# Performance work log

Hardware: AMD Instinct MI355X
Metric: run time of the kernel (lower is better)

Reference implementation:

```python
import jax, jax.numpy as jnp
import numpy as np

B, T, H, K = 64, 512, 768, 11
START_ID, END_ID = 9, 10  # tag_to_ix['<CLS>'], tag_to_ix['<SEP>']
NEG = -10000.0


def setup_inputs() -> dict:
    key = jax.random.key(0)
    k1, k2, k3, k4 = jax.random.split(key, 4)
    embeds = jax.random.normal(k1, (B, T, H), dtype=jnp.float32)
    W_fc = jax.random.normal(k2, (K, H), dtype=jnp.float32) * 0.02
    b_fc = jax.random.normal(k3, (K,), dtype=jnp.float32) * 0.02
    transitions = jax.random.normal(k4, (K, K), dtype=jnp.float32)
    # __init__ masking: no transition out of anything into START row, none into END col
    transitions = transitions.at[START_ID, :].set(NEG)
    transitions = transitions.at[:, END_ID].set(NEG)
    return {"embeds": embeds, "W_fc": W_fc, "b_fc": b_fc, "transitions": transitions}


def reference(embeds, W_fc, b_fc, transitions):
    # fc projection: feats[b,t,k] (PLM_crf path: encoder output -> Linear)
    feats = jnp.einsum('bth,kh->btk', embeds, W_fc) + b_fc  # [B,T,K]
    Bv, Tv, Kv = feats.shape

    # Viterbi: log_delta init -10000 except start tag; NOTE the original never
    # adds feats[:, 0] (loop starts at t=1), so we faithfully skip it too.
    log_delta0 = jnp.full((Bv, Kv), NEG, dtype=feats.dtype).at[:, START_ID].set(0.0)

    def step(log_delta, feat_t):
        # transitions[i, j]: score of moving from prev tag j to tag i
        scores = transitions[None, :, :] + log_delta[:, None, :]  # [B,K,K]
        psi_t = jnp.argmax(scores, axis=-1)                       # [B,K] best prev tag
        log_delta_new = jnp.max(scores, axis=-1) + feat_t         # [B,K]
        return log_delta_new, psi_t

    feats_seq = jnp.swapaxes(feats[:, 1:], 0, 1)                  # [T-1,B,K]
    log_delta, psi = jax.lax.scan(step, log_delta0, feats_seq)    # psi: [T-1,B,K]

    score = jnp.max(log_delta, axis=-1)                           # [B]
    last_tag = jnp.argmax(log_delta, axis=-1)                     # [B]

    # Backtrack: path[t] = psi[t+1][path[t+1]] for t = T-2 .. 0
    def back(next_tag, psi_t):
        tag = jnp.take_along_axis(psi_t, next_tag[:, None], axis=-1)[:, 0]
        return tag, tag

    _, path_rest = jax.lax.scan(back, last_tag, psi, reverse=True)  # [T-1,B]
    path = jnp.concatenate([jnp.swapaxes(path_rest, 0, 1), last_tag[:, None]], axis=1)  # [B,T]
    return score, path
```

## Files before the change

### kernel.cpp

```cpp
#include <hip/hip_runtime.h>

#define BB 64
#define TT 512
#define HH 768
#define KK 11
#define START_ID 9
#define NEGV -10000.0f
#define TT4 (TT + 4)
#define NROWS 16

typedef float vf2 __attribute__((ext_vector_type(2)));

__device__ __forceinline__ float ninf() { return __int_as_float(0xff800000); }

template <int CTRL>
__device__ __forceinline__ float dpp_add(float x) {
    int yi = __builtin_amdgcn_update_dpp(0, __float_as_int(x), CTRL, 0xF, 0xF, false);
    return x + __int_as_float(yi);
}

__device__ __forceinline__ float wave_sum_to_lane63(float x) {
    x = dpp_add<0x111>(x);
    x = dpp_add<0x112>(x);
    x = dpp_add<0x114>(x);
    x = dpp_add<0x118>(x);
    x = dpp_add<0x142>(x);
    x = dpp_add<0x143>(x);
    return x;
}

__device__ __forceinline__ float rlane(float v, int l) {
    return __int_as_float(__builtin_amdgcn_readlane(__float_as_int(v), l));
}

template <int PAT>
__device__ __forceinline__ float quad_fmax(float x) {
    int yi = __builtin_amdgcn_update_dpp(0, __float_as_int(x), PAT, 0xF, 0xF, false);
    return fmaxf(x, __int_as_float(yi));
}

__global__ __launch_bounds__(256) void fc_kernel(const float* __restrict__ embeds,
                                                 const float* __restrict__ W,
                                                 const float* __restrict__ bias,
                                                 float* __restrict__ feats) {
    __shared__ __align__(16) float w_lds[KK * HH];

    const int tid = threadIdx.x;
    const int lane = tid & 63;

    {
        const float4* src = reinterpret_cast<const float4*>(W);
        float4* dst = reinterpret_cast<float4*>(w_lds);
#pragma unroll
        for (int i = 0; i < 9; ++i) {
            int idx = tid + i * 256;
            if (idx < KK * HH / 4) dst[idx] = src[idx];
        }
    }

    float bk[KK];
#pragma unroll
    for (int k = 0; k < KK; ++k) bk[k] = bias[k];

    __syncthreads();

    const int wave_id = (blockIdx.x * blockDim.x + tid) >> 6;
    const int base = wave_id * 8;
    const int lo = lane * 4;

    const float* ea = embeds + (size_t)base * HH;
    const float* eb = ea + HH;
    float4 a0 = *reinterpret_cast<const float4*>(ea + 0   + lo);
    float4 a1 = *reinterpret_cast<const float4*>(ea + 256 + lo);
    float4 a2 = *reinterpret_cast<const float4*>(ea + 512 + lo);
    float4 b0 = *reinterpret_cast<const float4*>(eb + 0   + lo);
    float4 b1 = *reinterpret_cast<const float4*>(eb + 256 + lo);
    float4 b2 = *reinterpret_cast<const float4*>(eb + 512 + lo);

#pragma unroll 1
    for (int rr = 0; rr < 8; rr += 2) {
        const int nrr = (rr + 2) & 7;
        const float* na = embeds + (size_t)(base + nrr) * HH;
        const float* nb = na + HH;
        float4 na0 = *reinterpret_cast<const float4*>(na + 0   + lo);
        float4 na1 = *reinterpret_cast<const float4*>(na + 256 + lo);
        float4 na2 = *reinterpret_cast<const float4*>(na + 512 + lo);
        float4 nb0 = *reinterpret_cast<const float4*>(nb + 0   + lo);
        float4 nb1 = *reinterpret_cast<const float4*>(nb + 256 + lo);
        float4 nb2 = *reinterpret_cast<const float4*>(nb + 512 + lo);

        vf2 va[6] = {{a0.x, a0.y}, {a0.z, a0.w}, {a1.x, a1.y},
                     {a1.z, a1.w}, {a2.x, a2.y}, {a2.z, a2.w}};
        vf2 vb[6] = {{b0.x, b0.y}, {b0.z, b0.w}, {b1.x, b1.y},
                     {b1.z, b1.w}, {b2.x, b2.y}, {b2.z, b2.w}};

        float4 w0 = *reinterpret_cast<const float4*>(w_lds + 0 + lo);
        float4 w1 = *reinterpret_cast<const float4*>(w_lds + 256 + lo);
        float4 w2 = *reinterpret_cast<const float4*>(w_lds + 512 + lo);

        float rA[KK], rB[KK];
#pragma unroll
        for (int k = 0; k < KK; ++k) {
            const int nk = (k == KK - 1) ? 0 : k + 1;
            float4 nw0 = *reinterpret_cast<const float4*>(w_lds + nk * HH + 0 + lo);
            float4 nw1 = *reinterpret_cast<const float4*>(w_lds + nk * HH + 256 + lo);
            float4 nw2 = *reinterpret_cast<const float4*>(w_lds + nk * HH + 512 + lo);

            vf2 wv[6] = {{w0.x, w0.y}, {w0.z, w0.w},
                         {w1.x, w1.y}, {w1.z, w1.w},
                         {w2.x, w2.y}, {w2.z, w2.w}};
            vf2 sA = va[0] * wv[0];
            vf2 sB = vb[0] * wv[0];
#pragma unroll
            for (int r = 1; r < 6; ++r) { sA += va[r] * wv[r]; sB += vb[r] * wv[r]; }
            rA[k] = wave_sum_to_lane63(sA.x + sA.y);
            rB[k] = wave_sum_to_lane63(sB.x + sB.y);

            w0 = nw0; w1 = nw1; w2 = nw2;
        }

        if (lane == 63) {
            float* oA = feats + (size_t)(base + rr) * KK;
#pragma unroll
            for (int k = 0; k < KK; ++k) oA[k] = rA[k] + bk[k];
#pragma unroll
            for (int k = 0; k < KK; ++k) oA[KK + k] = rB[k] + bk[k];
        }

        a0 = na0; a1 = na1; a2 = na2;
        b0 = nb0; b1 = nb1; b2 = nb2;
    }
}

__global__ __launch_bounds__(256) void viterbi_kernel(const float* __restrict__ feats,
                                                      const float* __restrict__ trans,
                                                      float* __restrict__ out) {
    __shared__ __align__(16) float featsT[NROWS * TT4];
    __shared__ __align__(16) float dh[(TT - 1) * 12 + 16];
    __shared__ int psi_lds[(TT - 1) * KK];
    __shared__ float tr_lds[KK * KK];
    __shared__ int comp[15 * KK];
    __shared__ int bt[16];
    __shared__ int sh_last;

    const int tid = threadIdx.x;
    const int b = blockIdx.x;

    {
        const float4* src = reinterpret_cast<const float4*>(feats + (size_t)b * TT * KK);
        for (int idx4 = tid; idx4 < TT * KK / 4; idx4 += 256) {
            float4 v = src[idx4];
            const int e = idx4 * 4;
#pragma unroll
            for (int u = 0; u < 4; ++u) {
                int t = (e + u) / KK;
                int k = (e + u) - t * KK;
                if (t > 0) featsT[k * TT4 + (t - 1)] = (&v.x)[u];
            }
        }
        for (int x = tid; x < (NROWS - KK) * TT4; x += 256)
            featsT[KK * TT4 + x] = ninf();
        if (tid < KK * KK) tr_lds[tid] = trans[tid];
    }
    __syncthreads();

    if (tid < 64) {
        const int i = tid >> 2;
        const int q = tid & 3;

        float trq0, trq1, trq2;
        {
            const int j0 = 3 * q, j1 = 3 * q + 1, j2 = 3 * q + 2;
            trq0 = (i < KK && j0 < KK) ? tr_lds[i * KK + j0] : 0.0f;
            trq1 = (i < KK && j1 < KK) ? tr_lds[i * KK + j1] : 0.0f;
            trq2 = (i < KK && j2 < KK) ? tr_lds[i * KK + j2] : 0.0f;
        }
        const int a0 = 48 * q, a1 = 48 * q + 16, a2 = 48 * q + 32;

        float delta = (i == START_ID) ? 0.0f : ((i < KK) ? NEGV : ninf());

        auto vstep = [&](float fcur, float& hs) {
            hs = delta;
            const int di = __float_as_int(delta);
            float d0 = __int_as_float(__builtin_amdgcn_ds_bpermute(a0, di));
            float d1 = __int_as_float(__builtin_amdgcn_ds_bpermute(a1, di));
            float d2 = __int_as_float(__builtin_amdgcn_ds_bpermute(a2, di));
            float m = fmaxf(fmaxf(trq0 + d0, trq1 + d1), trq2 + d2);
            m = quad_fmax<0xB1>(m);
            m = quad_fmax<0x4E>(m);
            delta = m + fcur;
        };

        const float* frow = featsT + i * TT4;
        float* dwbase = dh + i;

        float h0, h1, h2, h3, h4, h5, h6, h7;
        float h8, h9, h10, h11, h12, h13, h14, h15;

        float4 A0 = *reinterpret_cast<const float4*>(frow + 0);
        float4 A1 = *reinterpret_cast<const float4*>(frow + 4);
        float4 A2 = *reinterpret_cast<const float4*>(frow + 8);
        float4 A3 = *reinterpret_cast<const float4*>(frow + 12);

#pragma unroll 1
        for (int c = 0; c < 31; ++c) {
            const float* nf = frow + (c + 1) * 16;
            float4 B0 = *reinterpret_cast<const float4*>(nf + 0);
            float4 B1 = *reinterpret_cast<const float4*>(nf + 4);
            float4 B2 = *reinterpret_cast<const float4*>(nf + 8);
            float4 B3 = *reinterpret_cast<const float4*>(nf + 12);

            vstep(A0.x, h0);  vstep(A0.y, h1);  vstep(A0.z, h2);  vstep(A0.w, h3);
            vstep(A1.x, h4);  vstep(A1.y, h5);  vstep(A1.z, h6);  vstep(A1.w, h7);
            vstep(A2.x, h8);  vstep(A2.y, h9);  vstep(A2.z, h10); vstep(A2.w, h11);
            vstep(A3.x, h12); vstep(A3.y, h13); vstep(A3.z, h14); vstep(A3.w, h15);

            if (q == 0 && i < KK) {
                float* dw = dwbase + c * 192;
                dw[0]   = h0;  dw[12]  = h1;  dw[24]  = h2;  dw[36]  = h3;
                dw[48]  = h4;  dw[60]  = h5;  dw[72]  = h6;  dw[84]  = h7;
                dw[96]  = h8;  dw[108] = h9;  dw[120] = h10; dw[132] = h11;
                dw[144] = h12; dw[156] = h13; dw[168] = h14; dw[180] = h15;
            }

            A0 = B0; A1 = B1; A2 = B2; A3 = B3;
        }
        vstep(A0.x, h0);  vstep(A0.y, h1);  vstep(A0.z, h2);  vstep(A0.w, h3);
        vstep(A1.x, h4);  vstep(A1.y, h5);  vstep(A1.z, h6);  vstep(A1.w, h7);
        vstep(A2.x, h8);  vstep(A2.y, h9);  vstep(A2.z, h10); vstep(A2.w, h11);
        vstep(A3.x, h12); vstep(A3.y, h13); vstep(A3.z, h14);
        if (q == 0 && i < KK) {
            float* dw = dwbase + 31 * 192;
            dw[0]   = h0;  dw[12]  = h1;  dw[24]  = h2;  dw[36]  = h3;
            dw[48]  = h4;  dw[60]  = h5;  dw[72]  = h6;  dw[84]  = h7;
            dw[96]  = h8;  dw[108] = h9;  dw[120] = h10; dw[132] = h11;
            dw[144] = h12; dw[156] = h13; dw[168] = h14;
        }

        float dfin[KK];
#pragma unroll
        for (int j = 0; j < KK; ++j) dfin[j] = rlane(delta, 4 * j);
        float best = dfin[0];
        int last = 0;
#pragma unroll
        for (int j = 1; j < KK; ++j) {
            bool c = dfin[j] > best;
            best = c ? dfin[j] : best;
            last = c ? j : last;
        }
        if (tid == 0) {
            out[b] = best;
            out[BB + (size_t)b * TT + (TT - 1)] = (float)last;
            sh_last = last;
        }
    }
    __syncthreads();

    {
        const int i = tid & 15;
        const int sg = tid >> 4;
        if (i < KK) {
            float tri[KK];
#pragma unroll
            for (int j = 0; j < KK; ++j) tri[j] = tr_lds[i * KK + j];
            for (int s = sg; s < TT - 1; s += 16) {
                const float4* dr = reinterpret_cast<const float4*>(dh + s * 12);
                float4 a = dr[0], c4 = dr[1], d4 = dr[2];
                float sc[KK] = {tri[0] + a.x,  tri[1] + a.y,  tri[2] + a.z,  tri[3] + a.w,
                                tri[4] + c4.x, tri[5] + c4.y, tri[6] + c4.z, tri[7] + c4.w,
                                tri[8] + d4.x, tri[9] + d4.y, tri[10] + d4.z};
                float bv = sc[0];
                int bj = 0;
#pragma unroll
                for (int j = 1; j < KK; ++j) {
                    bool c = sc[j] > bv;
                    bv = c ? sc[j] : bv;
                    bj = c ? j : bj;
                }
                psi_lds[s * KK + i] = bj;
            }
        }
    }
    __syncthreads();

    {
        const int c = tid >> 4;
        const int i = tid & 15;
        if (c < 15 && i < KK) {
            int cur = i;
            for (int s = c * 32 + 31; s >= c * 32; --s) cur = psi_lds[s * KK + cur];
            comp[c * KK + i] = cur;
        } else if (c == 15 && i == 0) {
            int cur = sh_last;
            float* po = out + BB + (size_t)b * TT;
            for (int s = TT - 2; s >= 480; --s) {
                cur = psi_lds[s * KK + cur];
                po[s] = (float)cur;
            }
            bt[15] = cur;
        }
    }
    __syncthreads();

    if (tid == 0) {
        for (int c = 14; c >= 1; --c) bt[c] = comp[c * KK + bt[c + 1]];
    }
    __syncthreads();

    if (tid < 15) {
        const int c = tid;
        int cur = bt[c + 1];
        float* po = out + BB + (size_t)b * TT;
        for (int s = c * 32 + 31; s >= c * 32; --s) {
            cur = psi_lds[s * KK + cur];
            po[s] = (float)cur;
        }
    }
}

extern "C" void kernel_launch(void* const* d_in, const int* in_sizes, int n_in,
                              void* d_out, int out_size, void* d_ws, size_t ws_size,
                              hipStream_t stream) {
    const float* embeds = (const float*)d_in[0];
    const float* W_fc   = (const float*)d_in[1];
    const float* b_fc   = (const float*)d_in[2];
    const float* trans  = (const float*)d_in[3];
    float* out = (float*)d_out;
    float* feats = (float*)d_ws;

    fc_kernel<<<1024, 256, 0, stream>>>(embeds, W_fc, b_fc, feats);
    viterbi_kernel<<<BB, 256, 0, stream>>>(feats, trans, out);
}
```

Before: 200.6 us.

## Split Viterbi into forward and backtrack kernels with DPP row-shuffle max

The forward recursion now handles four batch rows per wave: each 16-lane row covers one sequence, and the max over previous tags is built from 15 DPP row_shr shuffles instead of ds_bpermute plus quad reductions. Per-step deltas are written to a global workspace, and a separate backtrack kernel reloads them to rebuild psi and the path. The aim is shorter serial latency per step and fewer LDS permute round trips. In exchange the forward pass runs on only 16 blocks, adds an extra kernel launch, and moves delta history through global memory.

Measured after the change: 208.6 us. 4.0% more time.

```diff
diff --git a/kernel.cpp b/kernel.cpp
--- a/kernel.cpp
+++ b/kernel.cpp
@@ -7,11 +7,17 @@
 #define START_ID 9
 #define NEGV -10000.0f
 #define TT4 (TT + 4)
-#define NROWS 16
+#define DH_REAL ((TT - 1) * 12)
+#define DH_STRIDE 6144
 
 typedef float vf2 __attribute__((ext_vector_type(2)));
 
 __device__ __forceinline__ float ninf() { return __int_as_float(0xff800000); }
+
+template <int CTRL>
+__device__ __forceinline__ int dpp_i(int x) {
+    return __builtin_amdgcn_update_dpp(0, x, CTRL, 0xF, 0xF, false);
+}
 
 template <int CTRL>
 __device__ __forceinline__ float dpp_add(float x) {
@@ -31,12 +37,6 @@
 
 __device__ __forceinline__ float rlane(float v, int l) {
     return __int_as_float(__builtin_amdgcn_readlane(__float_as_int(v), l));
-}
-
-template <int PAT>
-__device__ __forceinline__ float quad_fmax(float x) {
-    int yi = __builtin_amdgcn_update_dpp(0, __float_as_int(x), PAT, 0xF, 0xF, false);
-    return fmaxf(x, __int_as_float(yi));
 }
 
 __global__ __launch_bounds__(256) void fc_kernel(const float* __restrict__ embeds,
@@ -132,22 +132,20 @@
     }
 }
 
-__global__ __launch_bounds__(256) void viterbi_kernel(const float* __restrict__ feats,
-                                                      const float* __restrict__ trans,
-                                                      float* __restrict__ out) {
-    __shared__ __align__(16) float featsT[NROWS * TT4];
-    __shared__ __align__(16) float dh[(TT - 1) * 12 + 16];
-    __shared__ int psi_lds[(TT - 1) * KK];
+__global__ __launch_bounds__(256) void vit_fwd(const float* __restrict__ feats,
+                                               const float* __restrict__ trans,
+                                               float* __restrict__ dh_g,
+                                               float* __restrict__ out) {
+    __shared__ __align__(16) float fT[45 * TT4];
     __shared__ float tr_lds[KK * KK];
-    __shared__ int comp[15 * KK];
-    __shared__ int bt[16];
-    __shared__ int sh_last;
+    __shared__ float sdelta[64];
 
     const int tid = threadIdx.x;
-    const int b = blockIdx.x;
-
-    {
-        const float4* src = reinterpret_cast<const float4*>(feats + (size_t)b * TT * KK);
+    const int g = blockIdx.x;
+
+    for (int bl = 0; bl < 4; ++bl) {
+        const float4* src = reinterpret_cast<const float4*>(feats + (size_t)(4 * g + bl) * TT * KK);
+        float* dstb = fT + bl * (KK * TT4);
         for (int idx4 = tid; idx4 < TT * KK / 4; idx4 += 256) {
             float4 v = src[idx4];
             const int e = idx4 * 4;
@@ -155,44 +153,67 @@
             for (int u = 0; u < 4; ++u) {
                 int t = (e + u) / KK;
                 int k = (e + u) - t * KK;
-                if (t > 0) featsT[k * TT4 + (t - 1)] = (&v.x)[u];
+                if (t > 0) dstb[k * TT4 + (t - 1)] = (&v.x)[u];
             }
         }
-        for (int x = tid; x < (NROWS - KK) * TT4; x += 256)
-            featsT[KK * TT4 + x] = ninf();
-        if (tid < KK * KK) tr_lds[tid] = trans[tid];
-    }
+    }
+    for (int x = tid; x < TT4; x += 256) fT[44 * TT4 + x] = ninf();
+    if (tid < KK * KK) tr_lds[tid] = trans[tid];
     __syncthreads();
 
     if (tid < 64) {
-        const int i = tid >> 2;
-        const int q = tid & 3;
-
-        float trq0, trq1, trq2;
+        const int j = tid & 15;
+        const int r = tid >> 4;
+        const int bb = 4 * g + r;
+
+        float cc[16];
         {
-            const int j0 = 3 * q, j1 = 3 * q + 1, j2 = 3 * q + 2;
-            trq0 = (i < KK && j0 < KK) ? tr_lds[i * KK + j0] : 0.0f;
-            trq1 = (i < KK && j1 < KK) ? tr_lds[i * KK + j1] : 0.0f;
-            trq2 = (i < KK && j2 < KK) ? tr_lds[i * KK + j2] : 0.0f;
-        }
-        const int a0 = 48 * q, a1 = 48 * q + 16, a2 = 48 * q + 32;
-
-        float delta = (i == START_ID) ? 0.0f : ((i < KK) ? NEGV : ninf());
+            const int probe = j;
+            int mr[16];
+            mr[0]  = j;
+            mr[1]  = dpp_i<0x121>(probe);  mr[2]  = dpp_i<0x122>(probe);
+            mr[3]  = dpp_i<0x123>(probe);  mr[4]  = dpp_i<0x124>(probe);
+            mr[5]  = dpp_i<0x125>(probe);  mr[6]  = dpp_i<0x126>(probe);
+            mr[7]  = dpp_i<0x127>(probe);  mr[8]  = dpp_i<0x128>(probe);
+            mr[9]  = dpp_i<0x129>(probe);  mr[10] = dpp_i<0x12A>(probe);
+            mr[11] = dpp_i<0x12B>(probe);  mr[12] = dpp_i<0x12C>(probe);
+            mr[13] = dpp_i<0x12D>(probe);  mr[14] = dpp_i<0x12E>(probe);
+            mr[15] = dpp_i<0x12F>(probe);
+#pragma unroll
+            for (int rr = 0; rr < 16; ++rr)
+                cc[rr] = (j < KK && mr[rr] < KK) ? tr_lds[j * KK + mr[rr]] : ninf();
+        }
+
+        float delta = (j == START_ID) ? 0.0f : ((j < KK) ? NEGV : ninf());
+
+        const float* frow = fT + ((j < KK) ? (r * KK + j) * TT4 : 44 * TT4);
+        float* dwbase = dh_g + (size_t)bb * DH_STRIDE + j;
 
         auto vstep = [&](float fcur, float& hs) {
             hs = delta;
             const int di = __float_as_int(delta);
-            float d0 = __int_as_float(__builtin_amdgcn_ds_bpermute(a0, di));
-            float d1 = __int_as_float(__builtin_amdgcn_ds_bpermute(a1, di));
-            float d2 = __int_as_float(__builtin_amdgcn_ds_bpermute(a2, di));
-            float m = fmaxf(fmaxf(trq0 + d0, trq1 + d1), trq2 + d2);
-            m = quad_fmax<0xB1>(m);
-            m = quad_fmax<0x4E>(m);
-            delta = m + fcur;
+            float tm0  = cc[0]  + delta;
+            float tm1  = cc[1]  + __int_as_float(dpp_i<0x121>(di));
+            float tm2  = cc[2]  + __int_as_float(dpp_i<0x122>(di));
+            float tm3  = cc[3]  + __int_as_float(dpp_i<0x123>(di));
+            float tm4  = cc[4]  + __int_as_float(dpp_i<0x124>(di));
+            float tm5  = cc[5]  + __int_as_float(dpp_i<0x125>(di));
+            float tm6  = cc[6]  + __int_as_float(dpp_i<0x126>(di));
+            float tm7  = cc[7]  + __int_as_float(dpp_i<0x127>(di));
+            float tm8  = cc[8]  + __int_as_float(dpp_i<0x128>(di));
+            float tm9  = cc[9]  + __int_as_float(dpp_i<0x129>(di));
+            float tm10 = cc[10] + __int_as_float(dpp_i<0x12A>(di));
+            float tm11 = cc[11] + __int_as_float(dpp_i<0x12B>(di));
+            float tm12 = cc[12] + __int_as_float(dpp_i<0x12C>(di));
+            float tm13 = cc[13] + __int_as_float(dpp_i<0x12D>(di));
+            float tm14 = cc[14] + __int_as_float(dpp_i<0x12E>(di));
+            float tm15 = cc[15] + __int_as_float(dpp_i<0x12F>(di));
+            float m0 = fmaxf(fmaxf(fmaxf(tm0, tm1), fmaxf(tm2, tm3)),
+                             fmaxf(fmaxf(tm4, tm5), fmaxf(tm6, tm7)));
+            float m1 = fmaxf(fmaxf(fmaxf(tm8, tm9), fmaxf(tm10, tm11)),
+                             fmaxf(fmaxf(tm12, tm13), fmaxf(tm14, tm15)));
+            delta = fmaxf(m0, m1) + fcur;
         };
-
-        const float* frow = featsT + i * TT4;
-        float* dwbase = dh + i;
 
         float h0, h1, h2, h3, h4, h5, h6, h7;
         float h8, h9, h10, h11, h12, h13, h14, h15;
@@ -215,7 +236,7 @@
             vstep(A2.x, h8);  vstep(A2.y, h9);  vstep(A2.z, h10); vstep(A2.w, h11);
             vstep(A3.x, h12); vstep(A3.y, h13); vstep(A3.z, h14); vstep(A3.w, h15);
 
-            if (q == 0 && i < KK) {
+            if (j < KK) {
                 float* dw = dwbase + c * 192;
                 dw[0]   = h0;  dw[12]  = h1;  dw[24]  = h2;  dw[36]  = h3;
                 dw[48]  = h4;  dw[60]  = h5;  dw[72]  = h6;  dw[84]  = h7;
@@ -229,7 +250,7 @@
         vstep(A1.x, h4);  vstep(A1.y, h5);  vstep(A1.z, h6);  vstep(A1.w, h7);
         vstep(A2.x, h8);  vstep(A2.y, h9);  vstep(A2.z, h10); vstep(A2.w, h11);
         vstep(A3.x, h12); vstep(A3.y, h13); vstep(A3.z, h14);
-        if (q == 0 && i < KK) {
+        if (j < KK) {
             float* dw = dwbase + 31 * 192;
             dw[0]   = h0;  dw[12]  = h1;  dw[24]  = h2;  dw[36]  = h3;
             dw[48]  = h4;  dw[60]  = h5;  dw[72]  = h6;  dw[84]  = h7;
@@ -237,22 +258,45 @@
             dw[144] = h12; dw[156] = h13; dw[168] = h14;
         }
 
-        float dfin[KK];
-#pragma unroll
-        for (int j = 0; j < KK; ++j) dfin[j] = rlane(delta, 4 * j);
-        float best = dfin[0];
+        sdelta[tid] = delta;
+    }
+    __syncthreads();
+
+    if (tid < 4) {
+        const int bb = 4 * g + tid;
+        float best = sdelta[tid * 16 + 0];
         int last = 0;
 #pragma unroll
-        for (int j = 1; j < KK; ++j) {
-            bool c = dfin[j] > best;
-            best = c ? dfin[j] : best;
-            last = c ? j : last;
-        }
-        if (tid == 0) {
-            out[b] = best;
-            out[BB + (size_t)b * TT + (TT - 1)] = (float)last;
-            sh_last = last;
-        }
+        for (int jj = 1; jj < KK; ++jj) {
+            float v = sdelta[tid * 16 + jj];
+            bool c = v > best;
+            best = c ? v : best;
+            last = c ? jj : last;
+        }
+        out[bb] = best;
+        out[BB + (size_t)bb * TT + (TT - 1)] = (float)last;
+    }
+}
+
+__global__ __launch_bounds__(256) void vit_back(const float* __restrict__ dh_g,
+                                                const float* __restrict__ trans,
+                                                float* __restrict__ out) {
+    __shared__ __align__(16) float dh[DH_REAL + 16];
+    __shared__ int psi_lds[(TT - 1) * KK];
+    __shared__ float tr_lds[KK * KK];
+    __shared__ int comp[15 * KK];
+    __shared__ int bt[16];
+    __shared__ int sh_last;
+
+    const int tid = threadIdx.x;
+    const int b = blockIdx.x;
+
+    {
+        const float4* src = reinterpret_cast<const float4*>(dh_g + (size_t)b * DH_STRIDE);
+        float4* dst = reinterpret_cast<float4*>(dh);
+        for (int idx = tid; idx < DH_REAL / 4; idx += 256) dst[idx] = src[idx];
+        if (tid < KK * KK) tr_lds[tid] = trans[tid];
+        if (tid == 0) sh_last = (int)out[BB + (size_t)b * TT + (TT - 1)];
     }
     __syncthreads();
 
@@ -327,7 +371,9 @@
     const float* trans  = (const float*)d_in[3];
     float* out = (float*)d_out;
     float* feats = (float*)d_ws;
+    float* dh_g  = (float*)((char*)d_ws + (size_t)BB * TT * KK * sizeof(float));
 
     fc_kernel<<<1024, 256, 0, stream>>>(embeds, W_fc, b_fc, feats);
-    viterbi_kernel<<<BB, 256, 0, stream>>>(feats, trans, out);
-}
+    vit_fwd<<<16, 256, 0, stream>>>(feats, trans, dh_g, out);
+    vit_back<<<BB, 256, 0, stream>>>(dh_g, trans, out);
+}
```
